# Performance work log

Hardware: AMD Instinct MI355X
Metric: run time of the kernel (lower is better)

## Reference

```python
import jax, jax.numpy as jnp
import numpy as np

N = 50000      # nodes
E = 800000     # edges (avg degree 16)
F_IN = 64      # node_feature_space
H = 64         # hidden_dim
G = 16         # graphs in batch
BN_EPS = 1e-5


def setup_inputs() -> dict:
    key = jax.random.key(0)
    ks = jax.random.split(key, 8)
    x = jax.random.normal(ks[0], (N, F_IN), jnp.float32)
    edge_index = jax.random.randint(ks[1], (2, E), 0, N, dtype=jnp.int64)
    batch = jnp.sort(jax.random.randint(ks[2], (N,), 0, G, dtype=jnp.int64))
    init = lambda k, shp, fan: jax.random.normal(k, shp, jnp.float32) / np.float32(np.sqrt(fan))
    params = dict(
        W1_0=init(ks[3], (F_IN, H), F_IN), b1_0=jnp.zeros((H,), jnp.float32),
        W2_0=init(ks[4], (H, H), H),       b2_0=jnp.zeros((H,), jnp.float32),
        g_0=jnp.ones((H,), jnp.float32),   be_0=jnp.zeros((H,), jnp.float32),
        W1_1=init(ks[5], (H, H), H),       b1_1=jnp.zeros((H,), jnp.float32),
        W2_1=init(ks[6], (H, H), H),       b2_1=jnp.zeros((H,), jnp.float32),
        g_1=jnp.ones((H,), jnp.float32),   be_1=jnp.zeros((H,), jnp.float32),
    )
    return dict(x=x, edge_index=edge_index, batch=batch, **params)


def _gin_layer(x, src, dst, W1, b1, W2, b2, g, be):
    # GINConv (eps=0): h_i = MLP(x_i + sum_{j->i} x_j)
    agg = jax.ops.segment_sum(x[src], dst, num_segments=N)   # [N, d]
    h = x + agg
    h = jnp.maximum(h @ W1 + b1, 0.0) @ W2 + b2              # Linear-ReLU-Linear
    # BatchNorm1d (training-mode batch stats, biased variance as in torch)
    mu = h.mean(axis=0)
    var = h.var(axis=0)
    h = (h - mu) * jax.lax.rsqrt(var + BN_EPS) * g + be
    return jnp.maximum(h, 0.0)                               # ReLU


def reference(x, edge_index, batch,
              W1_0, b1_0, W2_0, b2_0, g_0, be_0,
              W1_1, b1_1, W2_1, b2_1, g_1, be_1):
    src, dst = edge_index[0], edge_index[1]
    x = _gin_layer(x, src, dst, W1_0, b1_0, W2_0, b2_0, g_0, be_0)
    x = _gin_layer(x, src, dst, W1_1, b1_1, W2_1, b2_1, g_1, be_1)
    # global_mean_pool over graph ids
    cnt = jax.ops.segment_sum(jnp.ones((N,), x.dtype), batch, num_segments=G)
    sums = jax.ops.segment_sum(x, batch, num_segments=G)
    h_graph = sums / jnp.maximum(cnt, 1.0)[:, None]
    return (x, h_graph)
```

## Files before the change

### kernel.cpp

```cpp
#include <hip/hip_runtime.h>
#include <hip/hip_bf16.h>


constexpr int NN = 50000;
constexpr int NE = 800000;
constexpr int HD = 64;
constexpr int NG = 16;
constexpr float BN_EPS = 1e-5f;
constexpr int ROWCAP = 64;
constexpr int NPART = 8;
constexpr int PSZ = 6250;
constexpr int BR = 64;

__device__ __forceinline__ int rdl(int v, int l) {
    return __builtin_amdgcn_readlane(v, l);
}

__global__ __launch_bounds__(256)
void prep_kernel(const float* __restrict__ x, __hip_bfloat16* __restrict__ xb,
                 int* __restrict__ cnt, float* __restrict__ stats0,
                 float* __restrict__ stats1, float* __restrict__ psums) {
    int i4 = blockIdx.x * 256 + threadIdx.x;
    if (i4 < NN) cnt[i4] = 0;
    if (blockIdx.x == 0) {
        if (threadIdx.x < 128) stats0[threadIdx.x] = 0.f;
        else stats1[threadIdx.x - 128] = 0.f;
    } else if (blockIdx.x == 1) {
        *(float4*)(psums + threadIdx.x * 4) = make_float4(0.f, 0.f, 0.f, 0.f);
    }
    if (i4 >= NN * HD / 4) return;
    float4 v = *(const float4*)(x + (size_t)i4 * 4);
    union { ushort4 u; __hip_bfloat16 b[4]; } p;
    p.b[0] = __float2bfloat16(v.x);
    p.b[1] = __float2bfloat16(v.y);
    p.b[2] = __float2bfloat16(v.z);
    p.b[3] = __float2bfloat16(v.w);
    *(ushort4*)((unsigned short*)xb + (size_t)i4 * 4) = p.u;
}

__global__ __launch_bounds__(256)
void scatter_kernel(const int* __restrict__ ei, int* __restrict__ cnt,
                    unsigned short* __restrict__ csr) {
    int p = blockIdx.x & 7;
    int chunk = blockIdx.x >> 3;
    int e4 = (chunk * 256 + threadIdx.x) * 4;
    if (e4 >= NE) return;
    int4 s = *(const int4*)(ei + e4);
    int4 d = *(const int4*)(ei + NE + e4);
    int lo = p * PSZ, hi = lo + PSZ;
    int slot;
    if (d.x >= lo && d.x < hi) {
        slot = atomicAdd(&cnt[d.x], 1);
        if (slot < ROWCAP) csr[(d.x << 6) + slot] = (unsigned short)s.x;
    }
    if (d.y >= lo && d.y < hi) {
        slot = atomicAdd(&cnt[d.y], 1);
        if (slot < ROWCAP) csr[(d.y << 6) + slot] = (unsigned short)s.y;
    }
    if (d.z >= lo && d.z < hi) {
        slot = atomicAdd(&cnt[d.z], 1);
        if (slot < ROWCAP) csr[(d.z << 6) + slot] = (unsigned short)s.z;
    }
    if (d.w >= lo && d.w < hi) {
        slot = atomicAdd(&cnt[d.w], 1);
        if (slot < ROWCAP) csr[(d.w << 6) + slot] = (unsigned short)s.w;
    }
}

template <int MODE>
__global__ __launch_bounds__(1024)
void layer_kernel(const float* __restrict__ xin, const __hip_bfloat16* __restrict__ xg,
                  const int* __restrict__ cnt, const unsigned short* __restrict__ csr,
                  const float* __restrict__ stats_prev, const float* __restrict__ gp,
                  const float* __restrict__ bep,
                  const float* __restrict__ W1, const float* __restrict__ b1,
                  const float* __restrict__ W2, const float* __restrict__ b2,
                  float* __restrict__ hout, float* __restrict__ stats,
                  __hip_bfloat16* __restrict__ xbr) {
    __shared__ float sh[BR * 65];
    __shared__ float red[2][16][64];
    int tid = threadIdx.x;
    int base = blockIdx.x * BR;
    int w = tid >> 6, lane = tid & 63;
    int wu = __builtin_amdgcn_readfirstlane(w);

    float sc = 1.f, off = 0.f;
    if (MODE == 1) {
        const float inv = 1.f / (float)NN;
        float mu = stats_prev[lane] * inv;
        float var = stats_prev[64 + lane] * inv - mu * mu;
        sc = gp[lane] * rsqrtf(var + BN_EPS);
        off = bep[lane] - mu * sc;
    }

    for (int rl = wu * 4; rl < wu * 4 + 4; rl++) {
        int grow = base + rl;
        float acc = 0.f;
        if (grow < NN) {
            int m = min(cnt[grow], ROWCAP);
            int ids = (int)csr[((size_t)grow << 6) + lane];
            float sv = xin[(size_t)grow * HD + lane];
            acc = (MODE == 1) ? fmaxf(fmaf(sv, sc, off), 0.f) : sv;
            int j = 0;
            float a0 = 0.f, a1 = 0.f, a2 = 0.f, a3 = 0.f;
            float a4 = 0.f, a5 = 0.f, a6 = 0.f, a7 = 0.f;
            for (; j + 8 <= m; j += 8) {
                int n0 = rdl(ids, j);
                int n1 = rdl(ids, j + 1);
                int n2 = rdl(ids, j + 2);
                int n3 = rdl(ids, j + 3);
                int n4 = rdl(ids, j + 4);
                int n5 = rdl(ids, j + 5);
                int n6 = rdl(ids, j + 6);
                int n7 = rdl(ids, j + 7);
                float v0 = __bfloat162float(xg[((size_t)n0 << 6) + lane]);
                float v1 = __bfloat162float(xg[((size_t)n1 << 6) + lane]);
                float v2 = __bfloat162float(xg[((size_t)n2 << 6) + lane]);
                float v3 = __bfloat162float(xg[((size_t)n3 << 6) + lane]);
                float v4 = __bfloat162float(xg[((size_t)n4 << 6) + lane]);
                float v5 = __bfloat162float(xg[((size_t)n5 << 6) + lane]);
                float v6 = __bfloat162float(xg[((size_t)n6 << 6) + lane]);
                float v7 = __bfloat162float(xg[((size_t)n7 << 6) + lane]);
                if (MODE == 1) {
                    a0 += fmaxf(fmaf(v0, sc, off), 0.f);
                    a1 += fmaxf(fmaf(v1, sc, off), 0.f);
                    a2 += fmaxf(fmaf(v2, sc, off), 0.f);
                    a3 += fmaxf(fmaf(v3, sc, off), 0.f);
                    a4 += fmaxf(fmaf(v4, sc, off), 0.f);
                    a5 += fmaxf(fmaf(v5, sc, off), 0.f);
                    a6 += fmaxf(fmaf(v6, sc, off), 0.f);
                    a7 += fmaxf(fmaf(v7, sc, off), 0.f);
                } else {
                    a0 += v0; a1 += v1; a2 += v2; a3 += v3;
                    a4 += v4; a5 += v5; a6 += v6; a7 += v7;
                }
            }
            acc += ((a0 + a1) + (a2 + a3)) + ((a4 + a5) + (a6 + a7));
            for (; j < m; j++) {
                int nb = rdl(ids, j);
                float v = __bfloat162float(xg[((size_t)nb << 6) + lane]);
                acc += (MODE == 1) ? fmaxf(fmaf(v, sc, off), 0.f) : v;
            }
        }
        sh[rl * 65 + lane] = acc;
    }
    __syncthreads();

    float acc[4];
#pragma unroll
    for (int j = 0; j < 4; j++) acc[j] = b1[wu * 4 + j];
    for (int k = 0; k < 64; k++) {
        float a = sh[lane * 65 + k];
        float4 wv = *(const float4*)(W1 + k * 64 + wu * 4);
        acc[0] = fmaf(a, wv.x, acc[0]);
        acc[1] = fmaf(a, wv.y, acc[1]);
        acc[2] = fmaf(a, wv.z, acc[2]);
        acc[3] = fmaf(a, wv.w, acc[3]);
    }
    __syncthreads();

#pragma unroll
    for (int j = 0; j < 4; j++)
        sh[lane * 65 + wu * 4 + j] = fmaxf(acc[j], 0.f);
    __syncthreads();

#pragma unroll
    for (int j = 0; j < 4; j++) acc[j] = b2[wu * 4 + j];
    for (int k = 0; k < 64; k++) {
        float a = sh[lane * 65 + k];
        float4 wv = *(const float4*)(W2 + k * 64 + wu * 4);
        acc[0] = fmaf(a, wv.x, acc[0]);
        acc[1] = fmaf(a, wv.y, acc[1]);
        acc[2] = fmaf(a, wv.z, acc[2]);
        acc[3] = fmaf(a, wv.w, acc[3]);
    }
    __syncthreads();
#pragma unroll
    for (int j = 0; j < 4; j++)
        sh[lane * 65 + wu * 4 + j] = acc[j];
    __syncthreads();

    {
        int row = tid >> 4, col = (tid & 15) * 4;
        int grow = base + row;
        if (grow < NN) {
            const float* s = sh + row * 65 + col;
            float4 v = make_float4(s[0], s[1], s[2], s[3]);
            *(float4*)(hout + (size_t)grow * HD + col) = v;
            if (xbr) {
                union { ushort4 u; __hip_bfloat16 b[4]; } p;
                p.b[0] = __float2bfloat16(v.x);
                p.b[1] = __float2bfloat16(v.y);
                p.b[2] = __float2bfloat16(v.z);
                p.b[3] = __float2bfloat16(v.w);
                *(ushort4*)((unsigned short*)xbr + (size_t)grow * HD + col) = p.u;
            }
        }
    }

    {
        float s = 0.f, ss = 0.f;
#pragma unroll
        for (int r = 0; r < 4; r++) {
            int rl = wu * 4 + r;
            float v = (base + rl < NN) ? sh[rl * 65 + lane] : 0.f;
            s += v;
            ss += v * v;
        }
        red[0][wu][lane] = s;
        red[1][wu][lane] = ss;
        __syncthreads();
        if (tid < 64) {
            float S = 0.f;
#pragma unroll
            for (int q = 0; q < 16; q++) S += red[0][q][tid];
            atomicAdd(stats + tid, S);
        } else if (tid < 128) {
            int c = tid - 64;
            float SS = 0.f;
#pragma unroll
            for (int q = 0; q < 16; q++) SS += red[1][q][c];
            atomicAdd(stats + 64 + c, SS);
        }
    }
}

__global__ __launch_bounds__(256)
void norm_kernel(float* h, const float* __restrict__ stats,
                 const float* __restrict__ g, const float* __restrict__ be,
                 const int* __restrict__ batch, float* __restrict__ psums) {
    __shared__ float sg[2][64];
    if (threadIdx.x < 128) sg[threadIdx.x >> 6][threadIdx.x & 63] = 0.f;
    __syncthreads();
    size_t i4 = (size_t)blockIdx.x * 256 + threadIdx.x;
    int row = (int)(i4 >> 4);
    int base_row = blockIdx.x * 16;
    int g0 = batch[base_row];
    size_t off = i4 * 4;
    int col = (int)(off & 63);
    float4 v = *(const float4*)(h + off);
    float4 sm = *(const float4*)(stats + col);
    float4 sq = *(const float4*)(stats + 64 + col);
    float4 gg = *(const float4*)(g + col);
    float4 bb = *(const float4*)(be + col);
    const float inv = 1.f / (float)NN;
    float4 o;
    {
        float mu = sm.x * inv, var = sq.x * inv - mu * mu;
        float sc = gg.x * rsqrtf(var + BN_EPS);
        o.x = fmaxf((v.x - mu) * sc + bb.x, 0.f);
    }
    {
        float mu = sm.y * inv, var = sq.y * inv - mu * mu;
        float sc = gg.y * rsqrtf(var + BN_EPS);
        o.y = fmaxf((v.y - mu) * sc + bb.y, 0.f);
    }
    {
        float mu = sm.z * inv, var = sq.z * inv - mu * mu;
        float sc = gg.z * rsqrtf(var + BN_EPS);
        o.z = fmaxf((v.z - mu) * sc + bb.z, 0.f);
    }
    {
        float mu = sm.w * inv, var = sq.w * inv - mu * mu;
        float sc = gg.w * rsqrtf(var + BN_EPS);
        o.w = fmaxf((v.w - mu) * sc + bb.w, 0.f);
    }
    *(float4*)(h + off) = o;

    int dg = batch[row] - g0;
    if (dg <= 1) {
        atomicAdd(&sg[dg][col + 0], o.x);
        atomicAdd(&sg[dg][col + 1], o.y);
        atomicAdd(&sg[dg][col + 2], o.z);
        atomicAdd(&sg[dg][col + 3], o.w);
    } else {
        int gid = g0 + dg;
        atomicAdd(&psums[gid * HD + col + 0], o.x);
        atomicAdd(&psums[gid * HD + col + 1], o.y);
        atomicAdd(&psums[gid * HD + col + 2], o.z);
        atomicAdd(&psums[gid * HD + col + 3], o.w);
    }
    __syncthreads();
    if (threadIdx.x < 128) {
        int d = threadIdx.x >> 6;
        int c = threadIdx.x & 63;
        float s = sg[d][c];
        if (g0 + d < NG && s != 0.f) atomicAdd(&psums[(g0 + d) * HD + c], s);
    }
}

__device__ __forceinline__ int lower_bound_batch(const int* __restrict__ b, int val) {
    int lo = 0, hi = NN;
    while (lo < hi) {
        int mid = (lo + hi) >> 1;
        if (b[mid] < val) lo = mid + 1;
        else hi = mid;
    }
    return lo;
}

__global__ __launch_bounds__(1024)
void pool_finalize_kernel(const float* __restrict__ sums, const int* __restrict__ batch,
                          float* __restrict__ out) {
    int g = threadIdx.x >> 6;
    int col = threadIdx.x & 63;
    int s = lower_bound_batch(batch, g);
    int e = lower_bound_batch(batch, g + 1);
    float cnt = (float)(e - s);
    out[g * HD + col] = sums[g * HD + col] / fmaxf(cnt, 1.f);
}

extern "C" void kernel_launch(void* const* d_in, const int* in_sizes, int n_in,
                              void* d_out, int out_size, void* d_ws, size_t ws_size,
                              hipStream_t stream) {
    const float* x = (const float*)d_in[0];
    const int* ei = (const int*)d_in[1];
    const int* batch = (const int*)d_in[2];
    const float* W1_0 = (const float*)d_in[3];
    const float* b1_0 = (const float*)d_in[4];
    const float* W2_0 = (const float*)d_in[5];
    const float* b2_0 = (const float*)d_in[6];
    const float* g_0 = (const float*)d_in[7];
    const float* be_0 = (const float*)d_in[8];
    const float* W1_1 = (const float*)d_in[9];
    const float* b1_1 = (const float*)d_in[10];
    const float* W2_1 = (const float*)d_in[11];
    const float* b2_1 = (const float*)d_in[12];
    const float* g_1 = (const float*)d_in[13];
    const float* be_1 = (const float*)d_in[14];

    float* out = (float*)d_out;

    float* stats0 = (float*)d_ws;
    float* stats1 = stats0 + 128;
    float* psums = stats1 + 128;
    int* cnt = (int*)(psums + 1024);
    unsigned short* csr = (unsigned short*)(cnt + NN);
    __hip_bfloat16* xb = (__hip_bfloat16*)(csr + (size_t)NN * ROWCAP);
    __hip_bfloat16* xb2 = xb + (size_t)NN * HD;

    dim3 b256(256);
    dim3 b1024(1024);
    int layer_grid = (NN + BR - 1) / BR;
    int norm_grid = (NN * HD / 4 + 255) / 256;
    int sct_grid = ((NE + 1023) / 1024) * NPART;

    prep_kernel<<<norm_grid, b256, 0, stream>>>(x, xb, cnt, stats0, stats1, psums);
    scatter_kernel<<<sct_grid, b256, 0, stream>>>(ei, cnt, csr);

    layer_kernel<0><<<layer_grid, b1024, 0, stream>>>(
        x, xb, cnt, csr, nullptr, nullptr, nullptr,
        W1_0, b1_0, W2_0, b2_0, out, stats0, xb2);

    layer_kernel<1><<<layer_grid, b1024, 0, stream>>>(
        out, xb2, cnt, csr, stats0, g_0, be_0,
        W1_1, b1_1, W2_1, b2_1, out, stats1, (__hip_bfloat16*)nullptr);

    norm_kernel<<<norm_grid, b256, 0, stream>>>(out, stats1, g_1, be_1, batch, psums);
    pool_finalize_kernel<<<1, dim3(1024), 0, stream>>>(psums, batch, out + (size_t)NN * HD);
}
```

Measured before the change: 316.0 us.

## Fuse scatter, both GIN layers, norm and pooling into one persistent kernel

Replaces the scatter, two layer kernels, norm and pool-finalize launches with one persistent 1536-block kernel that uses a global atomic-counter barrier between phases. Gather and MLP are split into separate grid-stride phases with an intermediate bh buffer in global memory, and each block's MLP tile is computed by 4 waves holding 16 outputs each. This removes launch gaps and tail effects, at the cost of extra global traffic for the gathered activations, spin-barrier overhead, and a reliance on all 1536 blocks being co-resident.

```diff
diff --git a/kernel.cpp b/kernel.cpp
--- a/kernel.cpp
+++ b/kernel.cpp
@@ -10,16 +10,43 @@
 constexpr int ROWCAP = 64;
 constexpr int NPART = 8;
 constexpr int PSZ = 6250;
-constexpr int BR = 64;
+constexpr int GRID = 1536;
+constexpr int TPB = 256;
+constexpr int SCTV = ((NE + 1023) / 1024) * NPART;
+constexpr int MTILES = (NN + 63) / 64;
+constexpr int NORMV = NN / 16;
+constexpr int WPP = (GRID / NPART) * 4;
 
 __device__ __forceinline__ int rdl(int v, int l) {
     return __builtin_amdgcn_readlane(v, l);
+}
+
+__device__ __forceinline__ void devbar(unsigned int* ctr, unsigned int target) {
+    __syncthreads();
+    if (threadIdx.x == 0) {
+        __hip_atomic_fetch_add(ctr, 1u, __ATOMIC_RELEASE, __HIP_MEMORY_SCOPE_AGENT);
+        while (__hip_atomic_load(ctr, __ATOMIC_RELAXED, __HIP_MEMORY_SCOPE_AGENT) < target)
+            __builtin_amdgcn_s_sleep(8);
+        (void)__hip_atomic_load(ctr, __ATOMIC_ACQUIRE, __HIP_MEMORY_SCOPE_AGENT);
+    }
+    __syncthreads();
+}
+
+__device__ __forceinline__ int lower_bound_batch(const int* __restrict__ b, int val) {
+    int lo = 0, hi = NN;
+    while (lo < hi) {
+        int mid = (lo + hi) >> 1;
+        if (b[mid] < val) lo = mid + 1;
+        else hi = mid;
+    }
+    return lo;
 }
 
 __global__ __launch_bounds__(256)
 void prep_kernel(const float* __restrict__ x, __hip_bfloat16* __restrict__ xb,
                  int* __restrict__ cnt, float* __restrict__ stats0,
-                 float* __restrict__ stats1, float* __restrict__ psums) {
+                 float* __restrict__ stats1, float* __restrict__ psums,
+                 unsigned int* __restrict__ ctr) {
     int i4 = blockIdx.x * 256 + threadIdx.x;
     if (i4 < NN) cnt[i4] = 0;
     if (blockIdx.x == 0) {
@@ -27,6 +54,8 @@
         else stats1[threadIdx.x - 128] = 0.f;
     } else if (blockIdx.x == 1) {
         *(float4*)(psums + threadIdx.x * 4) = make_float4(0.f, 0.f, 0.f, 0.f);
+    } else if (blockIdx.x == 2 && threadIdx.x == 0) {
+        *ctr = 0u;
     }
     if (i4 >= NN * HD / 4) return;
     float4 v = *(const float4*)(x + (size_t)i4 * 4);
@@ -38,52 +67,18 @@
     *(ushort4*)((unsigned short*)xb + (size_t)i4 * 4) = p.u;
 }
 
-__global__ __launch_bounds__(256)
-void scatter_kernel(const int* __restrict__ ei, int* __restrict__ cnt,
-                    unsigned short* __restrict__ csr) {
+template <int MODE>
+__device__ void gather_phase(const float* __restrict__ xin,
+                             const __hip_bfloat16* __restrict__ xg,
+                             const int* __restrict__ cnt,
+                             const unsigned short* __restrict__ csr,
+                             const float* __restrict__ stats_prev,
+                             const float* __restrict__ gp,
+                             const float* __restrict__ bep,
+                             float* __restrict__ bh) {
+    int w = threadIdx.x >> 6, lane = threadIdx.x & 63;
     int p = blockIdx.x & 7;
-    int chunk = blockIdx.x >> 3;
-    int e4 = (chunk * 256 + threadIdx.x) * 4;
-    if (e4 >= NE) return;
-    int4 s = *(const int4*)(ei + e4);
-    int4 d = *(const int4*)(ei + NE + e4);
-    int lo = p * PSZ, hi = lo + PSZ;
-    int slot;
-    if (d.x >= lo && d.x < hi) {
-        slot = atomicAdd(&cnt[d.x], 1);
-        if (slot < ROWCAP) csr[(d.x << 6) + slot] = (unsigned short)s.x;
-    }
-    if (d.y >= lo && d.y < hi) {
-        slot = atomicAdd(&cnt[d.y], 1);
-        if (slot < ROWCAP) csr[(d.y << 6) + slot] = (unsigned short)s.y;
-    }
-    if (d.z >= lo && d.z < hi) {
-        slot = atomicAdd(&cnt[d.z], 1);
-        if (slot < ROWCAP) csr[(d.z << 6) + slot] = (unsigned short)s.z;
-    }
-    if (d.w >= lo && d.w < hi) {
-        slot = atomicAdd(&cnt[d.w], 1);
-        if (slot < ROWCAP) csr[(d.w << 6) + slot] = (unsigned short)s.w;
-    }
-}
-
-template <int MODE>
-__global__ __launch_bounds__(1024)
-void layer_kernel(const float* __restrict__ xin, const __hip_bfloat16* __restrict__ xg,
-                  const int* __restrict__ cnt, const unsigned short* __restrict__ csr,
-                  const float* __restrict__ stats_prev, const float* __restrict__ gp,
-                  const float* __restrict__ bep,
-                  const float* __restrict__ W1, const float* __restrict__ b1,
-                  const float* __restrict__ W2, const float* __restrict__ b2,
-                  float* __restrict__ hout, float* __restrict__ stats,
-                  __hip_bfloat16* __restrict__ xbr) {
-    __shared__ float sh[BR * 65];
-    __shared__ float red[2][16][64];
-    int tid = threadIdx.x;
-    int base = blockIdx.x * BR;
-    int w = tid >> 6, lane = tid & 63;
-    int wu = __builtin_amdgcn_readfirstlane(w);
-
+    int wg = (blockIdx.x >> 3) * 4 + w;
     float sc = 1.f, off = 0.f;
     if (MODE == 1) {
         const float inv = 1.f / (float)NN;
@@ -92,222 +87,303 @@
         sc = gp[lane] * rsqrtf(var + BN_EPS);
         off = bep[lane] - mu * sc;
     }
-
-    for (int rl = wu * 4; rl < wu * 4 + 4; rl++) {
-        int grow = base + rl;
-        float acc = 0.f;
-        if (grow < NN) {
-            int m = min(cnt[grow], ROWCAP);
-            int ids = (int)csr[((size_t)grow << 6) + lane];
-            float sv = xin[(size_t)grow * HD + lane];
-            acc = (MODE == 1) ? fmaxf(fmaf(sv, sc, off), 0.f) : sv;
-            int j = 0;
-            float a0 = 0.f, a1 = 0.f, a2 = 0.f, a3 = 0.f;
-            float a4 = 0.f, a5 = 0.f, a6 = 0.f, a7 = 0.f;
-            for (; j + 8 <= m; j += 8) {
-                int n0 = rdl(ids, j);
-                int n1 = rdl(ids, j + 1);
-                int n2 = rdl(ids, j + 2);
-                int n3 = rdl(ids, j + 3);
-                int n4 = rdl(ids, j + 4);
-                int n5 = rdl(ids, j + 5);
-                int n6 = rdl(ids, j + 6);
-                int n7 = rdl(ids, j + 7);
-                float v0 = __bfloat162float(xg[((size_t)n0 << 6) + lane]);
-                float v1 = __bfloat162float(xg[((size_t)n1 << 6) + lane]);
-                float v2 = __bfloat162float(xg[((size_t)n2 << 6) + lane]);
-                float v3 = __bfloat162float(xg[((size_t)n3 << 6) + lane]);
-                float v4 = __bfloat162float(xg[((size_t)n4 << 6) + lane]);
-                float v5 = __bfloat162float(xg[((size_t)n5 << 6) + lane]);
-                float v6 = __bfloat162float(xg[((size_t)n6 << 6) + lane]);
-                float v7 = __bfloat162float(xg[((size_t)n7 << 6) + lane]);
-                if (MODE == 1) {
-                    a0 += fmaxf(fmaf(v0, sc, off), 0.f);
-                    a1 += fmaxf(fmaf(v1, sc, off), 0.f);
-                    a2 += fmaxf(fmaf(v2, sc, off), 0.f);
-                    a3 += fmaxf(fmaf(v3, sc, off), 0.f);
-                    a4 += fmaxf(fmaf(v4, sc, off), 0.f);
-                    a5 += fmaxf(fmaf(v5, sc, off), 0.f);
-                    a6 += fmaxf(fmaf(v6, sc, off), 0.f);
-                    a7 += fmaxf(fmaf(v7, sc, off), 0.f);
-                } else {
-                    a0 += v0; a1 += v1; a2 += v2; a3 += v3;
-                    a4 += v4; a5 += v5; a6 += v6; a7 += v7;
+    int rend = (p + 1) * PSZ;
+    for (int r = p * PSZ + wg; r < rend; r += WPP) {
+        int m = min(cnt[r], ROWCAP);
+        int ids = (int)csr[((size_t)r << 6) + lane];
+        float sv = xin[(size_t)r * HD + lane];
+        float acc = (MODE == 1) ? fmaxf(fmaf(sv, sc, off), 0.f) : sv;
+        int j = 0;
+        float a0 = 0.f, a1 = 0.f, a2 = 0.f, a3 = 0.f;
+        float a4 = 0.f, a5 = 0.f, a6 = 0.f, a7 = 0.f;
+        for (; j + 8 <= m; j += 8) {
+            int n0 = rdl(ids, j);
+            int n1 = rdl(ids, j + 1);
+            int n2 = rdl(ids, j + 2);
+            int n3 = rdl(ids, j + 3);
+            int n4 = rdl(ids, j + 4);
+            int n5 = rdl(ids, j + 5);
+            int n6 = rdl(ids, j + 6);
+            int n7 = rdl(ids, j + 7);
+            float v0 = __bfloat162float(xg[((size_t)n0 << 6) + lane]);
+            float v1 = __bfloat162float(xg[((size_t)n1 << 6) + lane]);
+            float v2 = __bfloat162float(xg[((size_t)n2 << 6) + lane]);
+            float v3 = __bfloat162float(xg[((size_t)n3 << 6) + lane]);
+            float v4 = __bfloat162float(xg[((size_t)n4 << 6) + lane]);
+            float v5 = __bfloat162float(xg[((size_t)n5 << 6) + lane]);
+            float v6 = __bfloat162float(xg[((size_t)n6 << 6) + lane]);
+            float v7 = __bfloat162float(xg[((size_t)n7 << 6) + lane]);
+            if (MODE == 1) {
+                a0 += fmaxf(fmaf(v0, sc, off), 0.f);
+                a1 += fmaxf(fmaf(v1, sc, off), 0.f);
+                a2 += fmaxf(fmaf(v2, sc, off), 0.f);
+                a3 += fmaxf(fmaf(v3, sc, off), 0.f);
+                a4 += fmaxf(fmaf(v4, sc, off), 0.f);
+                a5 += fmaxf(fmaf(v5, sc, off), 0.f);
+                a6 += fmaxf(fmaf(v6, sc, off), 0.f);
+                a7 += fmaxf(fmaf(v7, sc, off), 0.f);
+            } else {
+                a0 += v0; a1 += v1; a2 += v2; a3 += v3;
+                a4 += v4; a5 += v5; a6 += v6; a7 += v7;
+            }
+        }
+        acc += ((a0 + a1) + (a2 + a3)) + ((a4 + a5) + (a6 + a7));
+        for (; j < m; j++) {
+            int nb = rdl(ids, j);
+            float v = __bfloat162float(xg[((size_t)nb << 6) + lane]);
+            acc += (MODE == 1) ? fmaxf(fmaf(v, sc, off), 0.f) : v;
+        }
+        bh[(size_t)r * HD + lane] = acc;
+    }
+}
+
+template <bool WRITE_XB>
+__device__ void mlp_phase(const float* __restrict__ bh,
+                          const float* __restrict__ W1, const float* __restrict__ b1,
+                          const float* __restrict__ W2, const float* __restrict__ b2,
+                          float* __restrict__ hout, float* __restrict__ stats,
+                          __hip_bfloat16* __restrict__ xbr,
+                          float* sh, float (*red)[4][64]) {
+    int tid = threadIdx.x;
+    int w = tid >> 6, lane = tid & 63;
+    int wu = __builtin_amdgcn_readfirstlane(w);
+    int cb = wu * 16;
+
+    for (int t = blockIdx.x; t < MTILES; t += GRID) {
+        int base = t * 64;
+#pragma unroll
+        for (int i = 0; i < 4; i++) {
+            int i4 = tid + 256 * i;
+            int row = i4 >> 4, col = (i4 & 15) * 4;
+            int grow = base + row;
+            float4 v = (grow < NN) ? *(const float4*)(bh + (size_t)grow * HD + col)
+                                   : make_float4(0.f, 0.f, 0.f, 0.f);
+            float* d = sh + row * 65 + col;
+            d[0] = v.x; d[1] = v.y; d[2] = v.z; d[3] = v.w;
+        }
+        __syncthreads();
+
+        float acc[16];
+#pragma unroll
+        for (int j = 0; j < 16; j++) acc[j] = b1[cb + j];
+        for (int k = 0; k < 64; k++) {
+            float a = sh[lane * 65 + k];
+            const float4* wr = (const float4*)(W1 + k * 64 + cb);
+#pragma unroll
+            for (int q = 0; q < 4; q++) {
+                float4 wv = wr[q];
+                acc[4 * q + 0] = fmaf(a, wv.x, acc[4 * q + 0]);
+                acc[4 * q + 1] = fmaf(a, wv.y, acc[4 * q + 1]);
+                acc[4 * q + 2] = fmaf(a, wv.z, acc[4 * q + 2]);
+                acc[4 * q + 3] = fmaf(a, wv.w, acc[4 * q + 3]);
+            }
+        }
+        __syncthreads();
+#pragma unroll
+        for (int j = 0; j < 16; j++)
+            sh[lane * 65 + cb + j] = fmaxf(acc[j], 0.f);
+        __syncthreads();
+
+#pragma unroll
+        for (int j = 0; j < 16; j++) acc[j] = b2[cb + j];
+        for (int k = 0; k < 64; k++) {
+            float a = sh[lane * 65 + k];
+            const float4* wr = (const float4*)(W2 + k * 64 + cb);
+#pragma unroll
+            for (int q = 0; q < 4; q++) {
+                float4 wv = wr[q];
+                acc[4 * q + 0] = fmaf(a, wv.x, acc[4 * q + 0]);
+                acc[4 * q + 1] = fmaf(a, wv.y, acc[4 * q + 1]);
+                acc[4 * q + 2] = fmaf(a, wv.z, acc[4 * q + 2]);
+                acc[4 * q + 3] = fmaf(a, wv.w, acc[4 * q + 3]);
+            }
+        }
+        __syncthreads();
+#pragma unroll
+        for (int j = 0; j < 16; j++)
+            sh[lane * 65 + cb + j] = acc[j];
+        __syncthreads();
+
+#pragma unroll
+        for (int i = 0; i < 4; i++) {
+            int i4 = tid + 256 * i;
+            int row = i4 >> 4, col = (i4 & 15) * 4;
+            int grow = base + row;
+            if (grow < NN) {
+                const float* s = sh + row * 65 + col;
+                float4 v = make_float4(s[0], s[1], s[2], s[3]);
+                *(float4*)(hout + (size_t)grow * HD + col) = v;
+                if (WRITE_XB) {
+                    union { ushort4 u; __hip_bfloat16 b[4]; } pk;
+                    pk.b[0] = __float2bfloat16(v.x);
+                    pk.b[1] = __float2bfloat16(v.y);
+                    pk.b[2] = __float2bfloat16(v.z);
+                    pk.b[3] = __float2bfloat16(v.w);
+                    *(ushort4*)((unsigned short*)xbr + (size_t)grow * HD + col) = pk.u;
                 }
             }
-            acc += ((a0 + a1) + (a2 + a3)) + ((a4 + a5) + (a6 + a7));
-            for (; j < m; j++) {
-                int nb = rdl(ids, j);
-                float v = __bfloat162float(xg[((size_t)nb << 6) + lane]);
-                acc += (MODE == 1) ? fmaxf(fmaf(v, sc, off), 0.f) : v;
-            }
-        }
-        sh[rl * 65 + lane] = acc;
-    }
-    __syncthreads();
-
-    float acc[4];
-#pragma unroll
-    for (int j = 0; j < 4; j++) acc[j] = b1[wu * 4 + j];
-    for (int k = 0; k < 64; k++) {
-        float a = sh[lane * 65 + k];
-        float4 wv = *(const float4*)(W1 + k * 64 + wu * 4);
-        acc[0] = fmaf(a, wv.x, acc[0]);
-        acc[1] = fmaf(a, wv.y, acc[1]);
-        acc[2] = fmaf(a, wv.z, acc[2]);
-        acc[3] = fmaf(a, wv.w, acc[3]);
-    }
-    __syncthreads();
-
-#pragma unroll
-    for (int j = 0; j < 4; j++)
-        sh[lane * 65 + wu * 4 + j] = fmaxf(acc[j], 0.f);
-    __syncthreads();
-
-#pragma unroll
-    for (int j = 0; j < 4; j++) acc[j] = b2[wu * 4 + j];
-    for (int k = 0; k < 64; k++) {
-        float a = sh[lane * 65 + k];
-        float4 wv = *(const float4*)(W2 + k * 64 + wu * 4);
-        acc[0] = fmaf(a, wv.x, acc[0]);
-        acc[1] = fmaf(a, wv.y, acc[1]);
-        acc[2] = fmaf(a, wv.z, acc[2]);
-        acc[3] = fmaf(a, wv.w, acc[3]);
-    }
-    __syncthreads();
-#pragma unroll
-    for (int j = 0; j < 4; j++)
-        sh[lane * 65 + wu * 4 + j] = acc[j];
-    __syncthreads();
+        }
+
+        {
+            float s = 0.f, ss = 0.f;
+#pragma unroll
+            for (int r = 0; r < 16; r++) {
+                int rl = wu * 16 + r;
+                float v = (base + rl < NN) ? sh[rl * 65 + lane] : 0.f;
+                s += v;
+                ss += v * v;
+            }
+            red[0][wu][lane] = s;
+            red[1][wu][lane] = ss;
+            __syncthreads();
+            if (tid < 64) {
+                float S = red[0][0][tid] + red[0][1][tid] + red[0][2][tid] + red[0][3][tid];
+                atomicAdd(stats + tid, S);
+            } else if (tid < 128) {
+                int c = tid - 64;
+                float SS = red[1][0][c] + red[1][1][c] + red[1][2][c] + red[1][3][c];
+                atomicAdd(stats + 64 + c, SS);
+            }
+        }
+    }
+}
+
+__global__ __launch_bounds__(256, 6)
+void gin_mega(const float* __restrict__ x, const int* __restrict__ ei,
+              const int* __restrict__ batch,
+              const float* __restrict__ W1_0, const float* __restrict__ b1_0,
+              const float* __restrict__ W2_0, const float* __restrict__ b2_0,
+              const float* __restrict__ g_0, const float* __restrict__ be_0,
+              const float* __restrict__ W1_1, const float* __restrict__ b1_1,
+              const float* __restrict__ W2_1, const float* __restrict__ b2_1,
+              const float* __restrict__ g_1, const float* __restrict__ be_1,
+              float* __restrict__ out, float* __restrict__ stats0,
+              float* __restrict__ stats1, float* __restrict__ psums,
+              int* __restrict__ cnt, unsigned short* __restrict__ csr,
+              __hip_bfloat16* __restrict__ xb, __hip_bfloat16* __restrict__ xb2,
+              float* __restrict__ bh, unsigned int* __restrict__ ctr) {
+    __shared__ float sh[64 * 65];
+    __shared__ float red[2][4][64];
+    int tid = threadIdx.x;
+    int bid = blockIdx.x;
+
+    for (int v = bid; v < SCTV; v += GRID) {
+        int p = v & 7;
+        int chunk = v >> 3;
+        int e4 = (chunk * 256 + tid) * 4;
+        if (e4 < NE) {
+            int4 s = *(const int4*)(ei + e4);
+            int4 d = *(const int4*)(ei + NE + e4);
+            int lo = p * PSZ, hi = lo + PSZ;
+            int slot;
+            if (d.x >= lo && d.x < hi) {
+                slot = atomicAdd(&cnt[d.x], 1);
+                if (slot < ROWCAP) csr[(d.x << 6) + slot] = (unsigned short)s.x;
+            }
+            if (d.y >= lo && d.y < hi) {
+                slot = atomicAdd(&cnt[d.y], 1);
+                if (slot < ROWCAP) csr[(d.y << 6) + slot] = (unsigned short)s.y;
+            }
+            if (d.z >= lo && d.z < hi) {
+                slot = atomicAdd(&cnt[d.z], 1);
+                if (slot < ROWCAP) csr[(d.z << 6) + slot] = (unsigned short)s.z;
+            }
+            if (d.w >= lo && d.w < hi) {
+                slot = atomicAdd(&cnt[d.w], 1);
+                if (slot < ROWCAP) csr[(d.w << 6) + slot] = (unsigned short)s.w;
+            }
+        }
+    }
+    devbar(ctr, 1u * GRID);
+
+    gather_phase<0>(x, xb, cnt, csr, nullptr, nullptr, nullptr, bh);
+    devbar(ctr, 2u * GRID);
+
+    mlp_phase<true>(bh, W1_0, b1_0, W2_0, b2_0, out, stats0, xb2, sh, red);
+    devbar(ctr, 3u * GRID);
+
+    gather_phase<1>(out, xb2, cnt, csr, stats0, g_0, be_0, bh);
+    devbar(ctr, 4u * GRID);
+
+    mlp_phase<false>(bh, W1_1, b1_1, W2_1, b2_1, out, stats1,
+                     (__hip_bfloat16*)nullptr, sh, red);
+    devbar(ctr, 5u * GRID);
 
     {
-        int row = tid >> 4, col = (tid & 15) * 4;
-        int grow = base + row;
-        if (grow < NN) {
-            const float* s = sh + row * 65 + col;
-            float4 v = make_float4(s[0], s[1], s[2], s[3]);
-            *(float4*)(hout + (size_t)grow * HD + col) = v;
-            if (xbr) {
-                union { ushort4 u; __hip_bfloat16 b[4]; } p;
-                p.b[0] = __float2bfloat16(v.x);
-                p.b[1] = __float2bfloat16(v.y);
-                p.b[2] = __float2bfloat16(v.z);
-                p.b[3] = __float2bfloat16(v.w);
-                *(ushort4*)((unsigned short*)xbr + (size_t)grow * HD + col) = p.u;
-            }
-        }
-    }
-
-    {
-        float s = 0.f, ss = 0.f;
-#pragma unroll
-        for (int r = 0; r < 4; r++) {
-            int rl = wu * 4 + r;
-            float v = (base + rl < NN) ? sh[rl * 65 + lane] : 0.f;
-            s += v;
-            ss += v * v;
-        }
-        red[0][wu][lane] = s;
-        red[1][wu][lane] = ss;
-        __syncthreads();
-        if (tid < 64) {
-            float S = 0.f;
-#pragma unroll
-            for (int q = 0; q < 16; q++) S += red[0][q][tid];
-            atomicAdd(stats + tid, S);
-        } else if (tid < 128) {
-            int c = tid - 64;
-            float SS = 0.f;
-#pragma unroll
-            for (int q = 0; q < 16; q++) SS += red[1][q][c];
-            atomicAdd(stats + 64 + c, SS);
-        }
-    }
-}
-
-__global__ __launch_bounds__(256)
-void norm_kernel(float* h, const float* __restrict__ stats,
-                 const float* __restrict__ g, const float* __restrict__ be,
-                 const int* __restrict__ batch, float* __restrict__ psums) {
-    __shared__ float sg[2][64];
-    if (threadIdx.x < 128) sg[threadIdx.x >> 6][threadIdx.x & 63] = 0.f;
-    __syncthreads();
-    size_t i4 = (size_t)blockIdx.x * 256 + threadIdx.x;
-    int row = (int)(i4 >> 4);
-    int base_row = blockIdx.x * 16;
-    int g0 = batch[base_row];
-    size_t off = i4 * 4;
-    int col = (int)(off & 63);
-    float4 v = *(const float4*)(h + off);
-    float4 sm = *(const float4*)(stats + col);
-    float4 sq = *(const float4*)(stats + 64 + col);
-    float4 gg = *(const float4*)(g + col);
-    float4 bb = *(const float4*)(be + col);
-    const float inv = 1.f / (float)NN;
-    float4 o;
-    {
-        float mu = sm.x * inv, var = sq.x * inv - mu * mu;
-        float sc = gg.x * rsqrtf(var + BN_EPS);
-        o.x = fmaxf((v.x - mu) * sc + bb.x, 0.f);
-    }
-    {
-        float mu = sm.y * inv, var = sq.y * inv - mu * mu;
-        float sc = gg.y * rsqrtf(var + BN_EPS);
-        o.y = fmaxf((v.y - mu) * sc + bb.y, 0.f);
-    }
-    {
-        float mu = sm.z * inv, var = sq.z * inv - mu * mu;
-        float sc = gg.z * rsqrtf(var + BN_EPS);
-        o.z = fmaxf((v.z - mu) * sc + bb.z, 0.f);
-    }
-    {
-        float mu = sm.w * inv, var = sq.w * inv - mu * mu;
-        float sc = gg.w * rsqrtf(var + BN_EPS);
-        o.w = fmaxf((v.w - mu) * sc + bb.w, 0.f);
-    }
-    *(float4*)(h + off) = o;
-
-    int dg = batch[row] - g0;
-    if (dg <= 1) {
-        atomicAdd(&sg[dg][col + 0], o.x);
-        atomicAdd(&sg[dg][col + 1], o.y);
-        atomicAdd(&sg[dg][col + 2], o.z);
-        atomicAdd(&sg[dg][col + 3], o.w);
-    } else {
-        int gid = g0 + dg;
-        atomicAdd(&psums[gid * HD + col + 0], o.x);
-        atomicAdd(&psums[gid * HD + col + 1], o.y);
-        atomicAdd(&psums[gid * HD + col + 2], o.z);
-        atomicAdd(&psums[gid * HD + col + 3], o.w);
-    }
-    __syncthreads();
-    if (threadIdx.x < 128) {
-        int d = threadIdx.x >> 6;
-        int c = threadIdx.x & 63;
-        float s = sg[d][c];
-        if (g0 + d < NG && s != 0.f) atomicAdd(&psums[(g0 + d) * HD + c], s);
-    }
-}
-
-__device__ __forceinline__ int lower_bound_batch(const int* __restrict__ b, int val) {
-    int lo = 0, hi = NN;
-    while (lo < hi) {
-        int mid = (lo + hi) >> 1;
-        if (b[mid] < val) lo = mid + 1;
-        else hi = mid;
-    }
-    return lo;
-}
-
-__global__ __launch_bounds__(1024)
-void pool_finalize_kernel(const float* __restrict__ sums, const int* __restrict__ batch,
-                          float* __restrict__ out) {
-    int g = threadIdx.x >> 6;
-    int col = threadIdx.x & 63;
-    int s = lower_bound_batch(batch, g);
-    int e = lower_bound_batch(batch, g + 1);
-    float cnt = (float)(e - s);
-    out[g * HD + col] = sums[g * HD + col] / fmaxf(cnt, 1.f);
+        float* sg = &red[0][0][0];
+        for (int nb = bid; nb < NORMV; nb += GRID) {
+            if (tid < 128) sg[tid] = 0.f;
+            __syncthreads();
+            size_t i4 = (size_t)nb * 256 + tid;
+            int rrow = (int)(i4 >> 4);
+            int base_row = nb * 16;
+            int g0 = batch[base_row];
+            size_t off = i4 * 4;
+            int col = (int)(off & 63);
+            float4 v = *(const float4*)(out + off);
+            float4 sm = *(const float4*)(stats1 + col);
+            float4 sq = *(const float4*)(stats1 + 64 + col);
+            float4 gg = *(const float4*)(g_1 + col);
+            float4 bb = *(const float4*)(be_1 + col);
+            const float inv = 1.f / (float)NN;
+            float4 o;
+            {
+                float mu = sm.x * inv, var = sq.x * inv - mu * mu;
+                float s = gg.x * rsqrtf(var + BN_EPS);
+                o.x = fmaxf((v.x - mu) * s + bb.x, 0.f);
+            }
+            {
+                float mu = sm.y * inv, var = sq.y * inv - mu * mu;
+                float s = gg.y * rsqrtf(var + BN_EPS);
+                o.y = fmaxf((v.y - mu) * s + bb.y, 0.f);
+            }
+            {
+                float mu = sm.z * inv, var = sq.z * inv - mu * mu;
+                float s = gg.z * rsqrtf(var + BN_EPS);
+                o.z = fmaxf((v.z - mu) * s + bb.z, 0.f);
+            }
+            {
+                float mu = sm.w * inv, var = sq.w * inv - mu * mu;
+                float s = gg.w * rsqrtf(var + BN_EPS);
+                o.w = fmaxf((v.w - mu) * s + bb.w, 0.f);
+            }
+            *(float4*)(out + off) = o;
+
+            int dg = batch[rrow] - g0;
+            if (dg <= 1) {
+                atomicAdd(&sg[dg * 64 + col + 0], o.x);
+                atomicAdd(&sg[dg * 64 + col + 1], o.y);
+                atomicAdd(&sg[dg * 64 + col + 2], o.z);
+                atomicAdd(&sg[dg * 64 + col + 3], o.w);
+            } else {
+                int gid = g0 + dg;
+                atomicAdd(&psums[gid * HD + col + 0], o.x);
+                atomicAdd(&psums[gid * HD + col + 1], o.y);
+                atomicAdd(&psums[gid * HD + col + 2], o.z);
+                atomicAdd(&psums[gid * HD + col + 3], o.w);
+            }
+            __syncthreads();
+            if (tid < 128) {
+                int d = tid >> 6;
+                int c = tid & 63;
+                float s = sg[d * 64 + c];
+                if (g0 + d < NG && s != 0.f) atomicAdd(&psums[(g0 + d) * HD + c], s);
+            }
+            __syncthreads();
+        }
+    }
+    devbar(ctr, 6u * GRID);
+
+    if (bid == 0) {
+        for (int idx = tid; idx < NG * HD; idx += TPB) {
+            int g = idx >> 6;
+            int col = idx & 63;
+            int s = lower_bound_batch(batch, g);
+            int e = lower_bound_batch(batch, g + 1);
+            float c = (float)(e - s);
+            out[(size_t)NN * HD + g * HD + col] = psums[g * HD + col] / fmaxf(c, 1.f);
+        }
+    }
 }
 
 extern "C" void kernel_launch(void* const* d_in, const int* in_sizes, int n_in,
@@ -334,28 +410,20 @@
     float* stats0 = (float*)d_ws;
     float* stats1 = stats0 + 128;
     float* psums = stats1 + 128;
-    int* cnt = (int*)(psums + 1024);
+    unsigned int* ctr = (unsigned int*)(psums + 1024);
+    int* cnt = (int*)(ctr + 16);
     unsigned short* csr = (unsigned short*)(cnt + NN);
     __hip_bfloat16* xb = (__hip_bfloat16*)(csr + (size_t)NN * ROWCAP);
     __hip_bfloat16* xb2 = xb + (size_t)NN * HD;
-
-    dim3 b256(256);
-    dim3 b1024(1024);
-    int layer_grid = (NN + BR - 1) / BR;
-    int norm_grid = (NN * HD / 4 + 255) / 256;
-    int sct_grid = ((NE + 1023) / 1024) * NPART;
-
-    prep_kernel<<<norm_grid, b256, 0, stream>>>(x, xb, cnt, stats0, stats1, psums);
-    scatter_kernel<<<sct_grid, b256, 0, stream>>>(ei, cnt, csr);
-
-    layer_kernel<0><<<layer_grid, b1024, 0, stream>>>(
-        x, xb, cnt, csr, nullptr, nullptr, nullptr,
-        W1_0, b1_0, W2_0, b2_0, out, stats0, xb2);
-
-    layer_kernel<1><<<layer_grid, b1024, 0, stream>>>(
-        out, xb2, cnt, csr, stats0, g_0, be_0,
-        W1_1, b1_1, W2_1, b2_1, out, stats1, (__hip_bfloat16*)nullptr);
-
-    norm_kernel<<<norm_grid, b256, 0, stream>>>(out, stats1, g_1, be_1, batch, psums);
-    pool_finalize_kernel<<<1, dim3(1024), 0, stream>>>(psums, batch, out + (size_t)NN * HD);
-}
+    float* bh = (float*)(xb2 + (size_t)NN * HD);
+
+    int prep_grid = (NN * HD / 4 + 255) / 256;
+
+    prep_kernel<<<prep_grid, dim3(256), 0, stream>>>(x, xb, cnt, stats0, stats1,
+                                                     psums, ctr);
+    gin_mega<<<GRID, dim3(TPB), 0, stream>>>(
+        x, ei, batch,
+        W1_0, b1_0, W2_0, b2_0, g_0, be_0,
+        W1_1, b1_1, W2_1, b2_1, g_1, be_1,
+        out, stats0, stats1, psums, cnt, csr, xb, xb2, bh, ctr);
+}
```

Measured after the change: 1.063 ms. +236.4%, slower.
